# Kernel optimization log

Measured on AMD Instinct MI355X. Metric: run time of the kernel, lower is better.

The kernel has to match this reference:

```python
import jax, jax.numpy as jnp
import numpy as np

N = 200000
E = 5000000


def _gcn_norm(edge_index, num_nodes):
    # add self-loops and compute symmetric normalization (PyG GCNConv default)
    loop = jnp.arange(num_nodes, dtype=edge_index.dtype)
    src = jnp.concatenate([edge_index[0], loop])
    dst = jnp.concatenate([edge_index[1], loop])
    ones = jnp.ones(dst.shape[0], dtype=jnp.float32)
    deg = jax.ops.segment_sum(ones, dst, num_segments=num_nodes)
    dis = jnp.where(deg > 0, jax.lax.rsqrt(deg), 0.0)
    norm = dis[src] * dis[dst]  # [E+N]
    return src, dst, norm


def _gcn_layer(x, src, dst, norm, W, b, num_nodes):
    xl = x @ W  # [N, out] dense linear (no bias, PyG default)
    msg = xl[src] * norm[:, None]  # gather + scale
    agg = jax.ops.segment_sum(msg, dst, num_segments=num_nodes)  # scatter-add
    return agg + b


def setup_inputs() -> dict:
    key = jax.random.key(0)
    ks = jax.random.split(key, 10)
    x = jax.random.normal(ks[0], (N, 12), dtype=jnp.float32)
    edge_index = jax.random.randint(ks[1], (2, E), 0, N, dtype=jnp.int64)
    def glorot(k, fi, fo):
        s = np.sqrt(6.0 / (fi + fo)).astype(np.float32)
        return jax.random.uniform(k, (fi, fo), jnp.float32, -s, s)
    return {
        "x": x,
        "edge_index": edge_index,
        "W1": glorot(ks[2], 12, 16), "b1": jnp.zeros((16,), jnp.float32),
        "W2": glorot(ks[3], 16, 8), "b2": jnp.zeros((8,), jnp.float32),
        "W3": glorot(ks[4], 8, 16), "b3": jnp.zeros((16,), jnp.float32),
        "W4": glorot(ks[5], 16, 12), "b4": jnp.zeros((12,), jnp.float32),
    }


def reference(x, edge_index, W1, b1, W2, b2, W3, b3, W4, b4):
    num_nodes = x.shape[0]
    src, dst, norm = _gcn_norm(edge_index, num_nodes)
    # Encoder
    h = jax.nn.relu(_gcn_layer(x, src, dst, norm, W1, b1, num_nodes))
    h = _gcn_layer(h, src, dst, norm, W2, b2, num_nodes)
    # Decoder
    h = jax.nn.relu(_gcn_layer(h, src, dst, norm, W3, b3, num_nodes))
    h = jax.nn.sigmoid(_gcn_layer(h, src, dst, norm, W4, b4, num_nodes))
    return h
```

## Files before the change

### kernel.cpp

```cpp
#include <hip/hip_runtime.h>
#include <hip/hip_fp16.h>
#include <math.h>


#define NPB 1024
#define MAX_NB 256
#define CAP 26496
#define BIN_CHUNK 4096
#define BIN_TH 512
#define EPT (BIN_CHUNK / BIN_TH)
#define MAXB CAP

__global__ void init_cur_kernel(int* __restrict__ bucket_cur, int NB) {
    int t = blockIdx.x * blockDim.x + threadIdx.x;
    if (t < NB) bucket_cur[t] = t * CAP;
}

__global__ __launch_bounds__(BIN_TH) void bin_kernel(const int* __restrict__ src,
                                                     const int* __restrict__ dst,
                                                     int* __restrict__ bucket_cur,
                                                     unsigned int* __restrict__ binned,
                                                     int E, int NB) {
    __shared__ int h[MAX_NB];
    __shared__ int scl[MAX_NB + 1];
    __shared__ int base[MAX_NB];
    __shared__ int sscan[256];
    __shared__ unsigned int stage[BIN_CHUNK];
    __shared__ unsigned char bkt8[BIN_CHUNK];
    int cbeg = blockIdx.x * BIN_CHUNK;
    int cend = min(cbeg + BIN_CHUNK, E);
    int chunk_n = cend - cbeg;
    int tid = threadIdx.x;

    for (int t = tid; t < NB; t += BIN_TH) h[t] = 0;
    __syncthreads();
    int myd[EPT];
#pragma unroll
    for (int j = 0; j < EPT; j++) {
        int e = cbeg + tid + j * BIN_TH;
        if (e < cend) {
            myd[j] = dst[e];
            atomicAdd(&h[myd[j] >> 10], 1);
        }
    }
    __syncthreads();
    int v = (tid < NB) ? h[tid] : 0;
    if (tid < 256) sscan[tid] = v;
    __syncthreads();
    for (int off = 1; off < 256; off <<= 1) {
        int t = (tid >= off && tid < 256) ? sscan[tid - off] : 0;
        __syncthreads();
        if (tid < 256) sscan[tid] += t;
        __syncthreads();
    }
    if (tid < NB) {
        scl[tid] = sscan[tid] - v;
        base[tid] = v ? atomicAdd(&bucket_cur[tid], v) : 0;
    }
    if (tid == 0) scl[NB] = chunk_n;
    __syncthreads();
    for (int t = tid; t < NB; t += BIN_TH) h[t] = 0;
    __syncthreads();
#pragma unroll
    for (int j = 0; j < EPT; j++) {
        int e = cbeg + tid + j * BIN_TH;
        if (e < cend) {
            int d = myd[j];
            int bkt = d >> 10;
            int pos = scl[bkt] + atomicAdd(&h[bkt], 1);
            stage[pos] = ((unsigned)src[e] << 10) | (unsigned)(d & 1023);
            bkt8[pos] = (unsigned char)bkt;
        }
    }
    __syncthreads();
    for (int k = tid; k < chunk_n; k += BIN_TH) {
        int bkt = bkt8[k];
        binned[base[bkt] + (k - scl[bkt])] = stage[k];
    }
}

__global__ __launch_bounds__(1024) void csr_bucket_kernel(
    const unsigned int* __restrict__ binned,
    const int* __restrict__ bucket_cur,
    int2* __restrict__ rows, float* __restrict__ dis,
    int* __restrict__ col, int N) {
    __shared__ int cnt[NPB];
    __shared__ int cur[NPB];
    __shared__ int colbuf[MAXB];
    int b = blockIdx.x;
    int nbase = b << 10;
    int nlocal = min(NPB, N - nbase);
    int beg = b * CAP;
    int bsize = bucket_cur[b] - beg;
    int tid = threadIdx.x;

    cnt[tid] = 0;
    __syncthreads();
    for (int k = tid; k < bsize; k += 1024)
        atomicAdd(&cnt[binned[beg + k] & 1023u], 1);
    __syncthreads();
    int v = cnt[tid];
    cur[tid] = v;
    __syncthreads();
    for (int off = 1; off < 1024; off <<= 1) {
        int t = (tid >= off) ? cur[tid - off] : 0;
        __syncthreads();
        cur[tid] += t;
        __syncthreads();
    }
    int excl = cur[tid] - v;
    if (tid < nlocal) {
        rows[nbase + tid] = make_int2(beg + excl, beg + excl + v);
        dis[nbase + tid] = 1.0f / sqrtf((float)(v + 1));
    }
    __syncthreads();
    cur[tid] = excl;
    __syncthreads();
    if (bsize <= MAXB) {
        for (int k = tid; k < bsize; k += 1024) {
            unsigned rec = binned[beg + k];
            int pos = atomicAdd(&cur[rec & 1023u], 1);
            colbuf[pos] = (int)(rec >> 10);
        }
        __syncthreads();
        for (int k = tid; k < bsize; k += 1024) col[beg + k] = colbuf[k];
    } else {
        for (int k = tid; k < bsize; k += 1024) {
            unsigned rec = binned[beg + k];
            int pos = atomicAdd(&cur[rec & 1023u], 1);
            col[beg + pos] = (int)(rec >> 10);
        }
    }
}

template <int IN, int OUT, int C, int PREACT, bool SPLITIN>
__global__ __launch_bounds__(256) void transform_kernel(
    const float* __restrict__ hin0, const float* __restrict__ hin1,
    const float* __restrict__ bias_prev,
    const float* __restrict__ W, const float* __restrict__ dis,
    __half* __restrict__ xls, int N) {
    __shared__ float sW[IN * OUT];
    __shared__ float sB[IN];
    for (int t = threadIdx.x; t < IN * OUT; t += blockDim.x) sW[t] = W[t];
    if (PREACT != 0) {
        for (int t = threadIdx.x; t < IN; t += blockDim.x) sB[t] = bias_prev[t];
    }
    __syncthreads();
    int i = blockIdx.x * blockDim.x + threadIdx.x;
    if (i >= N) return;

    constexpr int CIN = SPLITIN ? IN / 2 : IN;
    float h[IN];
#pragma unroll
    for (int k = 0; k < IN; k++) {
        float v;
        if (SPLITIN)
            v = (k < CIN) ? hin0[(size_t)i * CIN + k]
                          : hin1[(size_t)i * CIN + (k - CIN)];
        else
            v = hin0[(size_t)i * IN + k];
        if (PREACT != 0) {
            v += sB[k];
            if (PREACT == 1) v = fmaxf(v, 0.0f);
        }
        h[k] = v;
    }
    float d = dis[i];
    float o[OUT];
#pragma unroll
    for (int f = 0; f < OUT; f++) {
        float acc = 0.0f;
#pragma unroll
        for (int k = 0; k < IN; k++) acc = fmaf(h[k], sW[k * OUT + f], acc);
        o[f] = acc * d;
    }
    constexpr int NCH = OUT / C;
    constexpr int P = C / 2;
    __half2* x2 = (__half2*)xls;
#pragma unroll
    for (int c = 0; c < NCH; c++) {
#pragma unroll
        for (int k = 0; k < P; k++) {
            x2[(size_t)c * N * P + (size_t)i * P + k] =
                __floats2half2_rn(o[c * C + 2 * k], o[c * C + 2 * k + 1]);
        }
    }
}

template <int P>
__device__ __forceinline__ void acc_node(const __half2* __restrict__ x2, int c,
                                         float2 (&acc)[P]) {
    __half2 t[P];
#pragma unroll
    for (int k = 0; k < P; k++) t[k] = x2[(size_t)c * P + k];
#pragma unroll
    for (int k = 0; k < P; k++) {
        float2 v = __half22float2(t[k]);
        acc[k].x += v.x;
        acc[k].y += v.y;
    }
}

template <int P>
__device__ __forceinline__ void acc_quad(const __half2* __restrict__ x2, int4 c,
                                         float2 (&acc)[P]) {
    __half2 t[4][P];
#pragma unroll
    for (int k = 0; k < P; k++) t[0][k] = x2[(size_t)c.x * P + k];
#pragma unroll
    for (int k = 0; k < P; k++) t[1][k] = x2[(size_t)c.y * P + k];
#pragma unroll
    for (int k = 0; k < P; k++) t[2][k] = x2[(size_t)c.z * P + k];
#pragma unroll
    for (int k = 0; k < P; k++) t[3][k] = x2[(size_t)c.w * P + k];
#pragma unroll
    for (int k = 0; k < P; k++) {
        float2 a0 = __half22float2(t[0][k]), a1 = __half22float2(t[1][k]);
        float2 a2 = __half22float2(t[2][k]), a3 = __half22float2(t[3][k]);
        acc[k].x += (a0.x + a1.x) + (a2.x + a3.x);
        acc[k].y += (a0.y + a1.y) + (a2.y + a3.y);
    }
}

template <int C, bool SIG, int OST>
__device__ __forceinline__ void gather_body(
    int i, int p, const int2* __restrict__ rows, const int* __restrict__ col,
    const float* __restrict__ dis, const __half2* __restrict__ x2,
    float* __restrict__ outp, const float* __restrict__ bias, int coff) {
    constexpr int P = C / 2;
    float2 acc[P];
#pragma unroll
    for (int k = 0; k < P; k++) {
        if (p == 0) acc[k] = __half22float2(x2[(size_t)i * P + k]);
        else acc[k] = make_float2(0.0f, 0.0f);
    }
    int2 r = rows[i];
    int beg = r.x;
    int end = r.y;
    int nedge = end - beg;
    int pre = (4 - (beg & 3)) & 3;
    if (pre > nedge) pre = nedge;
    for (int j = p; j < pre; j += 2) acc_node<P>(x2, col[beg + j], acc);
    int abeg = beg + pre;
    int nq = (end - abeg) >> 2;
    int q = p;
    for (; q + 4 < nq; q += 6) {
        int4 ca = *reinterpret_cast<const int4*>(col + abeg + 4 * q);
        int4 cb = *reinterpret_cast<const int4*>(col + abeg + 4 * (q + 2));
        int4 cc = *reinterpret_cast<const int4*>(col + abeg + 4 * (q + 4));
        acc_quad<P>(x2, ca, acc);
        acc_quad<P>(x2, cb, acc);
        acc_quad<P>(x2, cc, acc);
    }
    for (; q < nq; q += 2) {
        int4 ca = *reinterpret_cast<const int4*>(col + abeg + 4 * q);
        acc_quad<P>(x2, ca, acc);
    }
    int tbeg = abeg + 4 * nq;
    for (int j = tbeg + p; j < end; j += 2) acc_node<P>(x2, col[j], acc);
#pragma unroll
    for (int k = 0; k < P; k++) {
        acc[k].x += __shfl_xor(acc[k].x, 1);
        acc[k].y += __shfl_xor(acc[k].y, 1);
    }
    float d = dis[i];
    float* op = outp + (size_t)i * OST + coff;
#pragma unroll
    for (int k = 0; k < P; k++) {
        if ((k & 1) == p) {
            float vx = acc[k].x * d;
            float vy = acc[k].y * d;
            if (SIG) {
                vx = 1.0f / (1.0f + expf(-(vx + bias[coff + 2 * k])));
                vy = 1.0f / (1.0f + expf(-(vy + bias[coff + 2 * k + 1])));
            }
            *reinterpret_cast<float2*>(op + 2 * k) = make_float2(vx, vy);
        }
    }
}

template <int C>
__global__ __launch_bounds__(256) void gather_kernel(
    const int2* __restrict__ rows, const int* __restrict__ col,
    const float* __restrict__ dis, const __half* __restrict__ xls,
    float* __restrict__ aggc, int N) {
    int tid = blockIdx.x * blockDim.x + threadIdx.x;
    int i = tid >> 1;
    int p = tid & 1;
    if (i >= N) return;
    gather_body<C, false, C>(i, p, rows, col, dis, (const __half2*)xls, aggc,
                             nullptr, 0);
}

template <int C>
__global__ __launch_bounds__(256) void gather2_kernel(
    const int2* __restrict__ rows, const int* __restrict__ col,
    const float* __restrict__ dis, const __half* __restrict__ x0,
    const __half* __restrict__ x1, float* __restrict__ agg0,
    float* __restrict__ agg1, int N) {
    int grp = blockIdx.x >> 3;
    int sub = blockIdx.x & 7;
    int chunk = sub >> 2;
    int range = (grp << 2) + (sub & 3);
    int t2 = range * 256 + (int)threadIdx.x;
    int i = t2 >> 1;
    int p = t2 & 1;
    if (i >= N) return;
    const __half2* x2 = (const __half2*)(chunk ? x1 : x0);
    float* aggc = chunk ? agg1 : agg0;
    gather_body<C, false, C>(i, p, rows, col, dis, x2, aggc, nullptr, 0);
}

__global__ __launch_bounds__(256) void gather2_sig_kernel(
    const int2* __restrict__ rows, const int* __restrict__ col,
    const float* __restrict__ dis, const __half* __restrict__ x0,
    const __half* __restrict__ x1, const float* __restrict__ bias,
    float* __restrict__ out, int N) {
    int grp = blockIdx.x >> 3;
    int sub = blockIdx.x & 7;
    int chunk = sub >> 2;
    int range = (grp << 2) + (sub & 3);
    int t2 = range * 256 + (int)threadIdx.x;
    int i = t2 >> 1;
    int p = t2 & 1;
    if (i >= N) return;
    const __half2* x2 = (const __half2*)(chunk ? x1 : x0);
    gather_body<6, true, 12>(i, p, rows, col, dis, x2, out, bias, chunk ? 6 : 0);
}

static inline size_t align_up(size_t v, size_t a) { return (v + a - 1) & ~(a - 1); }

extern "C" void kernel_launch(void* const* d_in, const int* in_sizes, int n_in,
                              void* d_out, int out_size, void* d_ws, size_t ws_size,
                              hipStream_t stream) {
    const float* x  = (const float*)d_in[0];
    const int*   ei = (const int*)d_in[1];
    const float* W1 = (const float*)d_in[2];
    const float* b1 = (const float*)d_in[3];
    const float* W2 = (const float*)d_in[4];
    const float* b2 = (const float*)d_in[5];
    const float* W3 = (const float*)d_in[6];
    const float* b3 = (const float*)d_in[7];
    const float* W4 = (const float*)d_in[8];
    const float* b4 = (const float*)d_in[9];
    float* out = (float*)d_out;

    const int N = in_sizes[0] / 12;
    const int E = in_sizes[1] / 2;
    const int* src = ei;
    const int* dst = ei + E;
    const int NB = (N + NPB - 1) / NPB;

    char* ws = (char*)d_ws;
    size_t off = 0;
    int* bucket_cur = (int*)(ws + off);   off = align_up(off + (size_t)NB * 4, 256);
    int2* rows = (int2*)(ws + off);       off = align_up(off + (size_t)N * 8, 256);
    float* dis = (float*)(ws + off);      off = align_up(off + (size_t)N * 4, 256);
    unsigned int* binned = (unsigned int*)(ws + off);
    off = align_up(off + ((size_t)NB * CAP + 4096) * 4, 256);
    int* col = (int*)(ws + off);          off = align_up(off + ((size_t)NB * CAP + 4096) * 4, 256);
    __half* xls = (__half*)(ws + off);    off = align_up(off + (size_t)N * 16 * 2, 256);
    float* aggA = (float*)(ws + off);     off = align_up(off + (size_t)N * 16 * 4, 256);
    float* aggB = (float*)(ws + off);     off = align_up(off + (size_t)N * 16 * 4, 256);
    (void)ws_size; (void)n_in; (void)out_size;

    const int B = 256;
    auto blocks = [&](long long n) { return (int)((n + B - 1) / B); };
    int nb2 = blocks(2LL * N);
    nb2 = (nb2 + 3) & ~3;
    const int G2 = nb2 * 2;

    init_cur_kernel<<<1, 256, 0, stream>>>(bucket_cur, NB);
    bin_kernel<<<(E + BIN_CHUNK - 1) / BIN_CHUNK, BIN_TH, 0, stream>>>(src, dst, bucket_cur, binned, E, NB);
    csr_bucket_kernel<<<NB, 1024, 0, stream>>>(binned, bucket_cur, rows, dis, col, N);

    __half* x_c0 = xls;
    __half* x_c8 = xls + (size_t)N * 8;
    __half* x_c6 = xls + (size_t)N * 6;
    float* aggA0 = aggA;
    float* aggA1 = aggA + (size_t)N * 8;
    float* aggB0 = aggB;

    transform_kernel<12, 16, 8, 0, false><<<blocks(N), B, 0, stream>>>(
        x, nullptr, nullptr, W1, dis, xls, N);
    gather2_kernel<8><<<G2, B, 0, stream>>>(rows, col, dis, x_c0, x_c8, aggA0, aggA1, N);

    transform_kernel<16, 8, 8, 1, true><<<blocks(N), B, 0, stream>>>(
        aggA0, aggA1, b1, W2, dis, xls, N);
    gather_kernel<8><<<blocks(2LL * N), B, 0, stream>>>(rows, col, dis, x_c0, aggB0, N);

    transform_kernel<8, 16, 8, 2, false><<<blocks(N), B, 0, stream>>>(
        aggB0, nullptr, b2, W3, dis, xls, N);
    gather2_kernel<8><<<G2, B, 0, stream>>>(rows, col, dis, x_c0, x_c8, aggA0, aggA1, N);

    transform_kernel<16, 12, 6, 1, true><<<blocks(N), B, 0, stream>>>(
        aggA0, aggA1, b3, W4, dis, xls, N);
    gather2_sig_kernel<<<G2, B, 0, stream>>>(rows, col, dis, x_c0, x_c6, b4, out, N);
}
```

Baseline: 408.5 us.

## Fuse first linear transform into CSR build and layer-3 transform into gather

```diff
diff --git a/kernel.cpp b/kernel.cpp
--- a/kernel.cpp
+++ b/kernel.cpp
@@ -79,14 +79,17 @@
     }
 }
 
-__global__ __launch_bounds__(1024) void csr_bucket_kernel(
+__global__ __launch_bounds__(1024) void csr_bucket_t1_kernel(
     const unsigned int* __restrict__ binned,
     const int* __restrict__ bucket_cur,
     int2* __restrict__ rows, float* __restrict__ dis,
-    int* __restrict__ col, int N) {
+    int* __restrict__ col,
+    const float* __restrict__ x, const float* __restrict__ W1,
+    __half* __restrict__ xls, int N) {
     __shared__ int cnt[NPB];
     __shared__ int cur[NPB];
     __shared__ int colbuf[MAXB];
+    __shared__ float sW[12 * 16];
     int b = blockIdx.x;
     int nbase = b << 10;
     int nlocal = min(NPB, N - nbase);
@@ -94,6 +97,7 @@
     int bsize = bucket_cur[b] - beg;
     int tid = threadIdx.x;
 
+    if (tid < 192) sW[tid] = W1[tid];
     cnt[tid] = 0;
     __syncthreads();
     for (int k = tid; k < bsize; k += 1024)
@@ -109,9 +113,10 @@
         __syncthreads();
     }
     int excl = cur[tid] - v;
+    float d = 1.0f / sqrtf((float)(v + 1));
     if (tid < nlocal) {
         rows[nbase + tid] = make_int2(beg + excl, beg + excl + v);
-        dis[nbase + tid] = 1.0f / sqrtf((float)(v + 1));
+        dis[nbase + tid] = d;
     }
     __syncthreads();
     cur[tid] = excl;
@@ -129,6 +134,29 @@
             unsigned rec = binned[beg + k];
             int pos = atomicAdd(&cur[rec & 1023u], 1);
             col[beg + pos] = (int)(rec >> 10);
+        }
+    }
+    if (tid < nlocal) {
+        int i = nbase + tid;
+        float h[12];
+#pragma unroll
+        for (int k = 0; k < 12; k++) h[k] = x[(size_t)i * 12 + k];
+        float o[16];
+#pragma unroll
+        for (int f = 0; f < 16; f++) {
+            float acc = 0.0f;
+#pragma unroll
+            for (int k = 0; k < 12; k++) acc = fmaf(h[k], sW[k * 16 + f], acc);
+            o[f] = acc * d;
+        }
+        __half2* x2 = (__half2*)xls;
+#pragma unroll
+        for (int c = 0; c < 2; c++) {
+#pragma unroll
+            for (int k = 0; k < 4; k++) {
+                x2[(size_t)c * N * 4 + (size_t)i * 4 + k] =
+                    __floats2half2_rn(o[c * 8 + 2 * k], o[c * 8 + 2 * k + 1]);
+            }
         }
     }
 }
@@ -222,13 +250,11 @@
     }
 }
 
-template <int C, bool SIG, int OST>
-__device__ __forceinline__ void gather_body(
+template <int C>
+__device__ __forceinline__ void gather_acc(
     int i, int p, const int2* __restrict__ rows, const int* __restrict__ col,
-    const float* __restrict__ dis, const __half2* __restrict__ x2,
-    float* __restrict__ outp, const float* __restrict__ bias, int coff) {
+    const __half2* __restrict__ x2, float2 (&acc)[C / 2]) {
     constexpr int P = C / 2;
-    float2 acc[P];
 #pragma unroll
     for (int k = 0; k < P; k++) {
         if (p == 0) acc[k] = __half22float2(x2[(size_t)i * P + k]);
@@ -263,33 +289,6 @@
         acc[k].x += __shfl_xor(acc[k].x, 1);
         acc[k].y += __shfl_xor(acc[k].y, 1);
     }
-    float d = dis[i];
-    float* op = outp + (size_t)i * OST + coff;
-#pragma unroll
-    for (int k = 0; k < P; k++) {
-        if ((k & 1) == p) {
-            float vx = acc[k].x * d;
-            float vy = acc[k].y * d;
-            if (SIG) {
-                vx = 1.0f / (1.0f + expf(-(vx + bias[coff + 2 * k])));
-                vy = 1.0f / (1.0f + expf(-(vy + bias[coff + 2 * k + 1])));
-            }
-            *reinterpret_cast<float2*>(op + 2 * k) = make_float2(vx, vy);
-        }
-    }
-}
-
-template <int C>
-__global__ __launch_bounds__(256) void gather_kernel(
-    const int2* __restrict__ rows, const int* __restrict__ col,
-    const float* __restrict__ dis, const __half* __restrict__ xls,
-    float* __restrict__ aggc, int N) {
-    int tid = blockIdx.x * blockDim.x + threadIdx.x;
-    int i = tid >> 1;
-    int p = tid & 1;
-    if (i >= N) return;
-    gather_body<C, false, C>(i, p, rows, col, dis, (const __half2*)xls, aggc,
-                             nullptr, 0);
 }
 
 template <int C>
@@ -298,6 +297,7 @@
     const float* __restrict__ dis, const __half* __restrict__ x0,
     const __half* __restrict__ x1, float* __restrict__ agg0,
     float* __restrict__ agg1, int N) {
+    constexpr int P = C / 2;
     int grp = blockIdx.x >> 3;
     int sub = blockIdx.x & 7;
     int chunk = sub >> 2;
@@ -308,7 +308,53 @@
     if (i >= N) return;
     const __half2* x2 = (const __half2*)(chunk ? x1 : x0);
     float* aggc = chunk ? agg1 : agg0;
-    gather_body<C, false, C>(i, p, rows, col, dis, x2, aggc, nullptr, 0);
+    float2 acc[P];
+    gather_acc<C>(i, p, rows, col, x2, acc);
+    float d = dis[i];
+    float2* ap = (float2*)(aggc + (size_t)i * C);
+#pragma unroll
+    for (int k = 0; k < P; k++) {
+        if ((k & 1) == p) ap[k] = make_float2(acc[k].x * d, acc[k].y * d);
+    }
+}
+
+__global__ __launch_bounds__(256) void gather_t3_kernel(
+    const int2* __restrict__ rows, const int* __restrict__ col,
+    const float* __restrict__ dis, const __half* __restrict__ xls,
+    const float* __restrict__ b2, const float* __restrict__ W3,
+    __half* __restrict__ xout, int N) {
+    __shared__ float sW[8 * 16];
+    __shared__ float sB[8];
+    if (threadIdx.x < 128) sW[threadIdx.x] = W3[threadIdx.x];
+    if (threadIdx.x < 8) sB[threadIdx.x] = b2[threadIdx.x];
+    __syncthreads();
+    int tid = blockIdx.x * blockDim.x + threadIdx.x;
+    int i = tid >> 1;
+    int p = tid & 1;
+    if (i >= N) return;
+    float2 acc[4];
+    gather_acc<8>(i, p, rows, col, (const __half2*)xls, acc);
+    float d = dis[i];
+    float v[8];
+#pragma unroll
+    for (int k = 0; k < 4; k++) {
+        v[2 * k] = acc[k].x * d + sB[2 * k];
+        v[2 * k + 1] = acc[k].y * d + sB[2 * k + 1];
+    }
+    float o[8];
+#pragma unroll
+    for (int f = 0; f < 8; f++) {
+        float a = 0.0f;
+#pragma unroll
+        for (int k = 0; k < 8; k++) a = fmaf(v[k], sW[k * 16 + p * 8 + f], a);
+        o[f] = a * d;
+    }
+    __half2* x2o = (__half2*)xout;
+#pragma unroll
+    for (int k = 0; k < 4; k++) {
+        x2o[(size_t)p * N * 4 + (size_t)i * 4 + k] =
+            __floats2half2_rn(o[2 * k], o[2 * k + 1]);
+    }
 }
 
 __global__ __launch_bounds__(256) void gather2_sig_kernel(
@@ -325,7 +371,19 @@
     int p = t2 & 1;
     if (i >= N) return;
     const __half2* x2 = (const __half2*)(chunk ? x1 : x0);
-    gather_body<6, true, 12>(i, p, rows, col, dis, x2, out, bias, chunk ? 6 : 0);
+    int coff = chunk ? 6 : 0;
+    float2 acc[3];
+    gather_acc<6>(i, p, rows, col, x2, acc);
+    float d = dis[i];
+    float* op = out + (size_t)i * 12 + coff;
+#pragma unroll
+    for (int k = 0; k < 3; k++) {
+        if ((k & 1) == p) {
+            float vx = 1.0f / (1.0f + expf(-(acc[k].x * d + bias[coff + 2 * k])));
+            float vy = 1.0f / (1.0f + expf(-(acc[k].y * d + bias[coff + 2 * k + 1])));
+            *reinterpret_cast<float2*>(op + 2 * k) = make_float2(vx, vy);
+        }
+    }
 }
 
 static inline size_t align_up(size_t v, size_t a) { return (v + a - 1) & ~(a - 1); }
@@ -360,8 +418,8 @@
     off = align_up(off + ((size_t)NB * CAP + 4096) * 4, 256);
     int* col = (int*)(ws + off);          off = align_up(off + ((size_t)NB * CAP + 4096) * 4, 256);
     __half* xls = (__half*)(ws + off);    off = align_up(off + (size_t)N * 16 * 2, 256);
+    __half* xls2 = (__half*)(ws + off);   off = align_up(off + (size_t)N * 16 * 2, 256);
     float* aggA = (float*)(ws + off);     off = align_up(off + (size_t)N * 16 * 4, 256);
-    float* aggB = (float*)(ws + off);     off = align_up(off + (size_t)N * 16 * 4, 256);
     (void)ws_size; (void)n_in; (void)out_size;
 
     const int B = 256;
@@ -372,28 +430,29 @@
 
     init_cur_kernel<<<1, 256, 0, stream>>>(bucket_cur, NB);
     bin_kernel<<<(E + BIN_CHUNK - 1) / BIN_CHUNK, BIN_TH, 0, stream>>>(src, dst, bucket_cur, binned, E, NB);
-    csr_bucket_kernel<<<NB, 1024, 0, stream>>>(binned, bucket_cur, rows, dis, col, N);
+    csr_bucket_t1_kernel<<<NB, 1024, 0, stream>>>(binned, bucket_cur, rows, dis, col,
+                                                  x, W1, xls, N);
 
     __half* x_c0 = xls;
     __half* x_c8 = xls + (size_t)N * 8;
     __half* x_c6 = xls + (size_t)N * 6;
+    __half* x2_c0 = xls2;
+    __half* x2_c8 = xls2 + (size_t)N * 8;
     float* aggA0 = aggA;
     float* aggA1 = aggA + (size_t)N * 8;
-    float* aggB0 = aggB;
-
-    transform_kernel<12, 16, 8, 0, false><<<blocks(N), B, 0, stream>>>(
-        x, nullptr, nullptr, W1, dis, xls, N);
+
     gather2_kernel<8><<<G2, B, 0, stream>>>(rows, col, dis, x_c0, x_c8, aggA0, aggA1, N);
 
     transform_kernel<16, 8, 8, 1, true><<<blocks(N), B, 0, stream>>>(
         aggA0, aggA1, b1, W2, dis, xls, N);
-    gather_kernel<8><<<blocks(2LL * N), B, 0, stream>>>(rows, col, dis, x_c0, aggB0, N);
-
-    transform_kernel<8, 16, 8, 2, false><<<blocks(N), B, 0, stream>>>(
-        aggB0, nullptr, b2, W3, dis, xls, N);
-    gather2_kernel<8><<<G2, B, 0, stream>>>(rows, col, dis, x_c0, x_c8, aggA0, aggA1, N);
+
+    gather_t3_kernel<<<blocks(2LL * N), B, 0, stream>>>(rows, col, dis, x_c0,
+                                                        b2, W3, xls2, N);
+
+    gather2_kernel<8><<<G2, B, 0, stream>>>(rows, col, dis, x2_c0, x2_c8, aggA0, aggA1, N);
 
     transform_kernel<16, 12, 6, 1, true><<<blocks(N), B, 0, stream>>>(
         aggA0, aggA1, b3, W4, dis, xls, N);
+
     gather2_sig_kernel<<<G2, B, 0, stream>>>(rows, col, dis, x_c0, x_c6, b4, out, N);
 }
```

Result: no change. 405.2 us (median of 2 runs) (-0.8%).
